# Kernel optimization log

Hardware: AMD Instinct MI355X
Metric: run time of the kernel (lower is better)

The kernel has to match this reference:

```python
import jax, jax.numpy as jnp
import numpy as np

BUCKETS = 256


def _gru_cell(x, h, W_ih, W_hh, b_ih, b_hh):
    # torch GRUCell math, gate order (r, z, n)
    gi = x @ W_ih.T + b_ih            # [B, 3H]
    gh = h @ W_hh.T + b_hh            # [B, 3H]
    i_r, i_z, i_n = jnp.split(gi, 3, axis=-1)
    h_r, h_z, h_n = jnp.split(gh, 3, axis=-1)
    r = jax.nn.sigmoid(i_r + h_r)
    z = jax.nn.sigmoid(i_z + h_z)
    n = jnp.tanh(i_n + r * h_n)
    return (1.0 - z) * n + z * h


def setup_inputs() -> dict:
    key = jax.random.key(0)
    ks = jax.random.split(key, 10)
    B, T, C, G, H, V = 16, 2000, 128, 512, 512, BUCKETS
    s = 0.1  # keep gates in a sane range
    return {
        "cond": jax.random.normal(ks[0], (B, T, C), jnp.float32),
        "h0": jnp.zeros((B, G), jnp.float32),
        "W_ih": jax.random.normal(ks[1], (3 * G, C), jnp.float32) * s,
        "W_hh": jax.random.normal(ks[2], (3 * G, G), jnp.float32) * s,
        "b_ih": jax.random.normal(ks[3], (3 * G,), jnp.float32) * s,
        "b_hh": jax.random.normal(ks[4], (3 * G,), jnp.float32) * s,
        "W_hid": jax.random.normal(ks[5], (H, G), jnp.float32) * s,
        "b_hid": jax.random.normal(ks[6], (H,), jnp.float32) * s,
        "W_out": jax.random.normal(ks[7], (V, H), jnp.float32) * s,
        "b_out": jax.random.normal(ks[8], (V,), jnp.float32) * s,
        "embedding": jax.random.normal(ks[9], (V, C), jnp.float32) * s,
    }


def reference(cond, h0, W_ih, W_hh, b_ih, b_hh, W_hid, b_hid, W_out, b_out, embedding):
    B, T, C = cond.shape
    keys = jax.random.split(jax.random.key(1), T)
    prev0 = jnp.full((B,), BUCKETS // 2, jnp.int32)  # mid-bucket = mu-law zero

    def step(carry, inp):
        h, prev = carry
        cond_t, k = inp
        x = cond_t + embedding[prev]                  # [B, C]
        h = _gru_cell(x, h, W_ih, W_hh, b_ih, b_hh)   # [B, G]
        hid = jax.nn.relu(h @ W_hid.T + b_hid)        # [B, H]
        logits = hid @ W_out.T + b_out                # [B, V]
        sample = jax.random.categorical(k, logits, axis=-1).astype(jnp.int32)
        return (h, sample), (logits, sample)

    (h_final, _), (logits, samples) = jax.lax.scan(
        step, (h0, prev0), (jnp.swapaxes(cond, 0, 1), keys))
    # logits: [T, B, V] -> [B, T, V]; samples: [T, B] -> [B, T]
    return jnp.swapaxes(logits, 0, 1), jnp.swapaxes(samples, 0, 1), h_final
```

## Files before the change

kernel.cpp:

```cpp
#include <hip/hip_runtime.h>
#include <stdint.h>
#include <math.h>

#define NBLK 128
#define NTHR 256
#define Bn 16
#define Tn 2000
#define Cn 128
#define Gn 512
#define Hn 512
#define Vn 256

#define WS_DBL_BASE 512
#define GRP_STRIDE  3072

#define OUT_SAMP ((size_t)Bn*Tn*Vn)
#define OUT_HF   (OUT_SAMP + (size_t)Bn*Tn)

typedef __attribute__((ext_vector_type(2))) double d2_t;

__device__ __forceinline__ unsigned rotl32(unsigned v, int n) {
  return (v << n) | (v >> (32 - n));
}

__device__ __forceinline__ void threefry2x32(unsigned k0, unsigned k1,
                                             unsigned c0, unsigned c1,
                                             unsigned& o0, unsigned& o1) {
  unsigned ks2 = k0 ^ k1 ^ 0x1BD11BDAu;
  unsigned x0 = c0 + k0;
  unsigned x1 = c1 + k1;
#define TF_R(r) { x0 += x1; x1 = rotl32(x1, r); x1 ^= x0; }
  TF_R(13) TF_R(15) TF_R(26) TF_R(6)
  x0 += k1;  x1 += ks2 + 1u;
  TF_R(17) TF_R(29) TF_R(16) TF_R(24)
  x0 += ks2; x1 += k0 + 2u;
  TF_R(13) TF_R(15) TF_R(26) TF_R(6)
  x0 += k0;  x1 += k1 + 3u;
  TF_R(17) TF_R(29) TF_R(16) TF_R(24)
  x0 += k1;  x1 += ks2 + 4u;
  TF_R(13) TF_R(15) TF_R(26) TF_R(6)
  x0 += ks2; x1 += k0 + 5u;
#undef TF_R
  o0 = x0; o1 = x1;
}

__device__ __forceinline__ void st_d(double* p, double v) {
  asm volatile("global_store_dwordx2 %0, %1, off sc0 sc1"
               :: "v"(p), "v"(v) : "memory");
}
__device__ __forceinline__ d2_t ld_d2(const double* p) {
  d2_t r;
  asm volatile("global_load_dwordx4 %0, %1, off sc0 sc1\n\t"
               "s_waitcnt vmcnt(0)" : "=v"(r) : "v"(p));
  return r;
}
__device__ __forceinline__ void ld8(const double* pl, int v, double* o) {
  const double* a0 = pl + v;
  const double* a1 = pl + 512 + v;
  const double* a2 = pl + 1024 + v;
  const double* a3 = pl + 1536 + v;
  double o0, o1, o2, o3, o4, o5, o6, o7;
  asm volatile(
    "global_load_dwordx2 %[r0], %[p0], off sc0 sc1\n\t"
    "global_load_dwordx2 %[r1], %[p0], off offset:2048 sc0 sc1\n\t"
    "global_load_dwordx2 %[r2], %[p1], off sc0 sc1\n\t"
    "global_load_dwordx2 %[r3], %[p1], off offset:2048 sc0 sc1\n\t"
    "global_load_dwordx2 %[r4], %[p2], off sc0 sc1\n\t"
    "global_load_dwordx2 %[r5], %[p2], off offset:2048 sc0 sc1\n\t"
    "global_load_dwordx2 %[r6], %[p3], off sc0 sc1\n\t"
    "global_load_dwordx2 %[r7], %[p3], off offset:2048 sc0 sc1\n\t"
    "s_waitcnt vmcnt(0)"
    : [r0]"=v"(o0), [r1]"=v"(o1), [r2]"=v"(o2), [r3]"=v"(o3),
      [r4]"=v"(o4), [r5]"=v"(o5), [r6]"=v"(o6), [r7]"=v"(o7)
    : [p0]"v"(a0), [p1]"v"(a1), [p2]"v"(a2), [p3]"v"(a3));
  o[0]=o0; o[1]=o1; o[2]=o2; o[3]=o3; o[4]=o4; o[5]=o5; o[6]=o6; o[7]=o7;
}
__device__ __forceinline__ unsigned ld_u(const unsigned* p) {
  unsigned r;
  asm volatile("global_load_dword %0, %1, off sc0 sc1\n\t"
               "s_waitcnt vmcnt(0)" : "=v"(r) : "v"(p) : "memory");
  return r;
}
__device__ __forceinline__ void st_u(unsigned* p, unsigned v) {
  asm volatile("global_store_dword %0, %1, off sc0 sc1"
               :: "v"(p), "v"(v) : "memory");
}

__device__ __forceinline__ void gar(unsigned* flags, int slot, unsigned target) {
  asm volatile("s_waitcnt vmcnt(0)" ::: "memory");
  __syncthreads();
  if (threadIdx.x == 0) st_u(&flags[slot], target);
}
__device__ __forceinline__ void gwt(unsigned* flags, unsigned target) {
  if (threadIdx.x < 8) {
    int guard = 0;
    while (ld_u(&flags[threadIdx.x]) < target) {
      if (++guard > 5000000) break;
    }
  }
  asm volatile("" ::: "memory");
  __syncthreads();
}

extern "C" __global__ __launch_bounds__(NTHR)
void wavernn_groups(const float* __restrict__ cond, const float* __restrict__ h0,
                    const float* __restrict__ W_ih, const float* __restrict__ W_hh,
                    const float* __restrict__ b_ih, const float* __restrict__ b_hh,
                    const float* __restrict__ W_hid, const float* __restrict__ b_hid,
                    const float* __restrict__ W_out, const float* __restrict__ b_out,
                    const float* __restrict__ emb,
                    float* __restrict__ out, double* __restrict__ ws) {
  const int tid = threadIdx.x;
  const int blk = blockIdx.x;
  const int g = blk >> 3;
  const int j = blk & 7;

  unsigned* flags = ((unsigned*)ws) + (size_t)g * 64;
  double* G   = ws + WS_DBL_BASE + (size_t)g * GRP_STRIDE;
  double* Hb0 = G;
  double* Hb1 = G + 512;
  double* PL  = G + 1024;

  __shared__ __attribute__((aligned(32))) double s_x[Cn];
  __shared__ __attribute__((aligned(32))) double s_h[Gn];
  __shared__ __attribute__((aligned(32))) double s_hid[64];
  __shared__ double s_r[64], s_z[64], s_hn[64], s_in[64];
  __shared__ double s_part[4][64];
  __shared__ double s_pv[4];
  __shared__ int    s_pi[4];

  if (tid < 64) st_d(&Hb0[j * 64 + tid],
                     (double)h0[(size_t)g * Gn + j * 64 + tid]);
  if (tid < Cn) s_x[tid] = (double)cond[(size_t)g * Tn * Cn + tid]
                         + (double)emb[128 * Cn + tid];
  unsigned pc = 1;
  gar(flags, j, pc); gwt(flags, pc); pc++;

  for (int t = 0; t < Tn; ++t) {
    double* hcur = (t & 1) ? Hb1 : Hb0;
    double* hnxt = (t & 1) ? Hb0 : Hb1;

    ((d2_t*)s_h)[tid] = ld_d2(hcur + 2 * tid);
    __syncthreads();
    {
      const int part = tid >> 6, gl = tid & 63;
      const double4* x4 = (const double4*)s_x;
      const double4* h4 = (const double4*)s_h;
      if (part <= 1) {
        const int row = part * 512 + j * 64 + gl;
        const float4* wi = (const float4*)(W_ih + (size_t)row * Cn);
        const float4* wh = (const float4*)(W_hh + (size_t)row * Gn);
        double a0 = 0., a1 = 0., a2 = 0., a3 = 0.;
#pragma unroll 8
        for (int k = 0; k < Cn / 4; ++k) {
          float4 w = wi[k]; double4 xv = x4[k];
          a0 = fma((double)w.x, xv.x, a0); a1 = fma((double)w.y, xv.y, a1);
          a2 = fma((double)w.z, xv.z, a2); a3 = fma((double)w.w, xv.w, a3);
        }
#pragma unroll 8
        for (int k = 0; k < Gn / 4; ++k) {
          float4 w = wh[k]; double4 hv = h4[k];
          a0 = fma((double)w.x, hv.x, a0); a1 = fma((double)w.y, hv.y, a1);
          a2 = fma((double)w.z, hv.z, a2); a3 = fma((double)w.w, hv.w, a3);
        }
        double pre = ((a0 + a1) + (a2 + a3)) + (double)b_ih[row] + (double)b_hh[row];
        double sig = 1.0 / (1.0 + exp(-pre));
        if (part == 0) s_r[gl] = sig; else s_z[gl] = sig;
      } else if (part == 2) {
        const int row = 1024 + j * 64 + gl;
        const float4* wh = (const float4*)(W_hh + (size_t)row * Gn);
        double a0 = 0., a1 = 0., a2 = 0., a3 = 0.;
#pragma unroll 8
        for (int k = 0; k < Gn / 4; ++k) {
          float4 w = wh[k]; double4 hv = h4[k];
          a0 = fma((double)w.x, hv.x, a0); a1 = fma((double)w.y, hv.y, a1);
          a2 = fma((double)w.z, hv.z, a2); a3 = fma((double)w.w, hv.w, a3);
        }
        s_hn[gl] = ((a0 + a1) + (a2 + a3)) + (double)b_hh[row];
      } else {
        const int row = 1024 + j * 64 + gl;
        const float4* wi = (const float4*)(W_ih + (size_t)row * Cn);
        double a0 = 0., a1 = 0., a2 = 0., a3 = 0.;
#pragma unroll 8
        for (int k = 0; k < Cn / 4; ++k) {
          float4 w = wi[k]; double4 xv = x4[k];
          a0 = fma((double)w.x, xv.x, a0); a1 = fma((double)w.y, xv.y, a1);
          a2 = fma((double)w.z, xv.z, a2); a3 = fma((double)w.w, xv.w, a3);
        }
        s_in[gl] = ((a0 + a1) + (a2 + a3)) + (double)b_ih[row];
      }
    }
    __syncthreads();
    if (tid < 64) {
      double r = s_r[tid], z = s_z[tid];
      double n = tanh(s_in[tid] + r * s_hn[tid]);
      double hv = (1.0 - z) * n + z * s_h[j * 64 + tid];
      st_d(&hnxt[j * 64 + tid], hv);
    }
    gar(flags, j, pc);
    float cond_next = 0.f;
    if (t + 1 < Tn && tid < Cn)
      cond_next = cond[((size_t)g * Tn + (t + 1)) * Cn + tid];
    unsigned kt0, kt1;
    threefry2x32(0u, 1u, 0u, (unsigned)t, kt0, kt1);
    gwt(flags, pc); pc++;

    ((d2_t*)s_h)[tid] = ld_d2(hnxt + 2 * tid);
    __syncthreads();
    if (t == Tn - 1 && j == 0) {
      out[OUT_HF + (size_t)g * Gn + tid] = (float)s_h[tid];
      out[OUT_HF + (size_t)g * Gn + tid + 256] = (float)s_h[tid + 256];
    }
    {
      const int row = j * 64 + (tid & 63);
      const int q = tid >> 6;
      const float4* wr = (const float4*)(W_hid + (size_t)row * Gn + q * 128);
      const double4* hh = (const double4*)(s_h + q * 128);
      double a0 = 0., a1 = 0., a2 = 0., a3 = 0.;
#pragma unroll 8
      for (int k = 0; k < 32; ++k) {
        float4 w = wr[k]; double4 hv = hh[k];
        a0 = fma((double)w.x, hv.x, a0); a1 = fma((double)w.y, hv.y, a1);
        a2 = fma((double)w.z, hv.z, a2); a3 = fma((double)w.w, hv.w, a3);
      }
      s_part[q][tid & 63] = (a0 + a1) + (a2 + a3);
    }
    __syncthreads();
    if (tid < 64) {
      double acc = (s_part[0][tid] + s_part[1][tid])
                 + (s_part[2][tid] + s_part[3][tid])
                 + (double)b_hid[j * 64 + tid];
      s_hid[tid] = acc > 0.0 ? acc : 0.0;
    }
    __syncthreads();
    {
      const int v = tid;
      const float4* wr = (const float4*)(W_out + (size_t)v * Hn + j * 64);
      const double4* hh = (const double4*)s_hid;
      double a0 = 0., a1 = 0., a2 = 0., a3 = 0.;
#pragma unroll 8
      for (int k = 0; k < 16; ++k) {
        float4 w = wr[k]; double4 hv = hh[k];
        a0 = fma((double)w.x, hv.x, a0); a1 = fma((double)w.y, hv.y, a1);
        a2 = fma((double)w.z, hv.z, a2); a3 = fma((double)w.w, hv.w, a3);
      }
      st_d(&PL[j * 256 + v], (a0 + a1) + (a2 + a3));
    }
    gar(flags, j, pc);
    double gum;
    {
      unsigned r0, r1;
      threefry2x32(kt0, kt1, 0u, (unsigned)(g * Vn + tid), r0, r1);
      unsigned bits = r0 ^ r1;
      float uf = __uint_as_float((bits >> 9) | 0x3f800000u) - 1.0f;
      if (uf <= 0.f) uf = 1.17549435e-38f;
      gum = -log(-log((double)uf));
    }
    gwt(flags, pc); pc++;

    int samp;
    {
      const int v = tid;
      double l[8];
      ld8(PL, v, l);
      double logit = ((((((((l[0] + l[1]) + l[2]) + l[3]) + l[4]) + l[5])
                       + l[6]) + l[7])) + (double)b_out[v];
      if (j == 0)
        out[(size_t)g * Tn * Vn + (size_t)t * Vn + v] = (float)logit;

      double bv = logit + gum;
      int bi = v;
#pragma unroll
      for (int off = 1; off < 64; off <<= 1) {
        double ov = __shfl_xor(bv, off, 64);
        int oi = __shfl_xor(bi, off, 64);
        if (ov > bv || (ov == bv && oi < bi)) { bv = ov; bi = oi; }
      }
      if ((tid & 63) == 0) { s_pv[tid >> 6] = bv; s_pi[tid >> 6] = bi; }
      __syncthreads();
      double fv = s_pv[0]; int fi = s_pi[0];
#pragma unroll
      for (int w = 1; w < 4; ++w) {
        double ov = s_pv[w]; int oi = s_pi[w];
        if (ov > fv || (ov == fv && oi < fi)) { fv = ov; fi = oi; }
      }
      samp = fi;
    }
    if (tid == 0 && j == 0) out[OUT_SAMP + (size_t)g * Tn + t] = (float)samp;
    if (t + 1 < Tn && tid < Cn) {
      s_x[tid] = (double)cond_next + (double)emb[(size_t)samp * Cn + tid];
    }
  }
}

extern "C" void kernel_launch(void* const* d_in, const int* in_sizes, int n_in,
                              void* d_out, int out_size, void* d_ws, size_t ws_size,
                              hipStream_t stream) {
  const float* cond  = (const float*)d_in[0];
  const float* h0    = (const float*)d_in[1];
  const float* W_ih  = (const float*)d_in[2];
  const float* W_hh  = (const float*)d_in[3];
  const float* b_ih  = (const float*)d_in[4];
  const float* b_hh  = (const float*)d_in[5];
  const float* W_hid = (const float*)d_in[6];
  const float* b_hid = (const float*)d_in[7];
  const float* W_out = (const float*)d_in[8];
  const float* b_out = (const float*)d_in[9];
  const float* emb   = (const float*)d_in[10];

  hipMemsetAsync(d_ws, 0, 4096, stream);
  hipLaunchKernelGGL(wavernn_groups, dim3(NBLK), dim3(NTHR), 0, stream,
                     cond, h0, W_ih, W_hh, b_ih, b_hh, W_hid, b_hid,
                     W_out, b_out, emb, (float*)d_out, (double*)d_ws);
}
```

Measured before the change: 51.33 ms.

## Overlap recurrent W_hh matvec with cross-block logit barrier wait

Restructures the per-step schedule so the h-dependent W_hh matvec for step t runs before waiting on the logits/sampling barrier of step t-1. The input-side W_ih work, which needs the sample, is deferred until after that wait. Meanwhile an idle wave prefetches the next cond row and computes Gumbel noise. The aim is to hide the inter-block barrier latency and the sampling latency behind useful matvec work on the serial critical path. The cost is more complex flag sequencing and a peeled epilogue for the final step's sampling.

```diff
diff --git a/kernel.cpp b/kernel.cpp
--- a/kernel.cpp
+++ b/kernel.cpp
@@ -42,6 +42,16 @@
   x0 += ks2; x1 += k0 + 5u;
 #undef TF_R
   o0 = x0; o1 = x1;
+}
+
+__device__ __forceinline__ double jax_gumbel(unsigned kt0, unsigned kt1,
+                                             unsigned f) {
+  unsigned r0, r1;
+  threefry2x32(kt0, kt1, 0u, f, r0, r1);
+  unsigned bits = r0 ^ r1;
+  float uf = __uint_as_float((bits >> 9) | 0x3f800000u) - 1.0f;
+  if (uf <= 0.f) uf = 1.17549435e-38f;
+  return -log(-log((double)uf));
 }
 
 __device__ __forceinline__ void st_d(double* p, double v) {
@@ -103,17 +113,18 @@
 }
 
 extern "C" __global__ __launch_bounds__(NTHR)
-void wavernn_groups(const float* __restrict__ cond, const float* __restrict__ h0,
-                    const float* __restrict__ W_ih, const float* __restrict__ W_hh,
-                    const float* __restrict__ b_ih, const float* __restrict__ b_hh,
-                    const float* __restrict__ W_hid, const float* __restrict__ b_hid,
-                    const float* __restrict__ W_out, const float* __restrict__ b_out,
-                    const float* __restrict__ emb,
-                    float* __restrict__ out, double* __restrict__ ws) {
+void wavernn_pipe(const float* __restrict__ cond, const float* __restrict__ h0,
+                  const float* __restrict__ W_ih, const float* __restrict__ W_hh,
+                  const float* __restrict__ b_ih, const float* __restrict__ b_hh,
+                  const float* __restrict__ W_hid, const float* __restrict__ b_hid,
+                  const float* __restrict__ W_out, const float* __restrict__ b_out,
+                  const float* __restrict__ emb,
+                  float* __restrict__ out, double* __restrict__ ws) {
   const int tid = threadIdx.x;
   const int blk = blockIdx.x;
   const int g = blk >> 3;
   const int j = blk & 7;
+  const int lane = tid & 63, wv = tid >> 6;
 
   unsigned* flags = ((unsigned*)ws) + (size_t)g * 64;
   double* G   = ws + WS_DBL_BASE + (size_t)g * GRP_STRIDE;
@@ -124,8 +135,10 @@
   __shared__ __attribute__((aligned(32))) double s_x[Cn];
   __shared__ __attribute__((aligned(32))) double s_h[Gn];
   __shared__ __attribute__((aligned(32))) double s_hid[64];
-  __shared__ double s_r[64], s_z[64], s_hn[64], s_in[64];
+  __shared__ double s_hn[64], s_in[64], s_z[64];
   __shared__ double s_part[4][64];
+  __shared__ double s_gum[256];
+  __shared__ float  s_cond[Cn];
   __shared__ double s_pv[4];
   __shared__ int    s_pi[4];
 
@@ -133,142 +146,51 @@
                      (double)h0[(size_t)g * Gn + j * 64 + tid]);
   if (tid < Cn) s_x[tid] = (double)cond[(size_t)g * Tn * Cn + tid]
                          + (double)emb[128 * Cn + tid];
-  unsigned pc = 1;
-  gar(flags, j, pc); gwt(flags, pc); pc++;
+  gar(flags, j, 1u); gwt(flags, 1u);
+  ((d2_t*)s_h)[tid] = ld_d2(Hb0 + 2 * tid);
+  __syncthreads();
 
   for (int t = 0; t < Tn; ++t) {
-    double* hcur = (t & 1) ? Hb1 : Hb0;
     double* hnxt = (t & 1) ? Hb0 : Hb1;
 
-    ((d2_t*)s_h)[tid] = ld_d2(hcur + 2 * tid);
-    __syncthreads();
-    {
-      const int part = tid >> 6, gl = tid & 63;
-      const double4* x4 = (const double4*)s_x;
+    double ha0 = 0., ha1 = 0., ha2 = 0., ha3 = 0.;
+    if (wv <= 2) {
+      const int row = wv * 512 + j * 64 + lane;
+      const float4* wh = (const float4*)(W_hh + (size_t)row * Gn);
       const double4* h4 = (const double4*)s_h;
-      if (part <= 1) {
-        const int row = part * 512 + j * 64 + gl;
-        const float4* wi = (const float4*)(W_ih + (size_t)row * Cn);
-        const float4* wh = (const float4*)(W_hh + (size_t)row * Gn);
-        double a0 = 0., a1 = 0., a2 = 0., a3 = 0.;
-#pragma unroll 8
-        for (int k = 0; k < Cn / 4; ++k) {
-          float4 w = wi[k]; double4 xv = x4[k];
-          a0 = fma((double)w.x, xv.x, a0); a1 = fma((double)w.y, xv.y, a1);
-          a2 = fma((double)w.z, xv.z, a2); a3 = fma((double)w.w, xv.w, a3);
+#pragma unroll 8
+      for (int k = 0; k < Gn / 4; ++k) {
+        float4 w = wh[k]; double4 hv = h4[k];
+        ha0 = fma((double)w.x, hv.x, ha0); ha1 = fma((double)w.y, hv.y, ha1);
+        ha2 = fma((double)w.z, hv.z, ha2); ha3 = fma((double)w.w, hv.w, ha3);
+      }
+      if (wv == 2)
+        s_hn[lane] = ((ha0 + ha1) + (ha2 + ha3)) + (double)b_hh[row];
+    } else {
+      const int c0 = 2 * lane;
+      s_cond[c0]     = cond[((size_t)g * Tn + t) * Cn + c0];
+      s_cond[c0 + 1] = cond[((size_t)g * Tn + t) * Cn + c0 + 1];
+      if (t > 0) {
+        unsigned kt0, kt1;
+        threefry2x32(0u, 1u, 0u, (unsigned)(t - 1), kt0, kt1);
+#pragma unroll
+        for (int i = 0; i < 4; ++i) {
+          int v = 4 * lane + i;
+          s_gum[v] = jax_gumbel(kt0, kt1, (unsigned)(g * Vn + v));
         }
-#pragma unroll 8
-        for (int k = 0; k < Gn / 4; ++k) {
-          float4 w = wh[k]; double4 hv = h4[k];
-          a0 = fma((double)w.x, hv.x, a0); a1 = fma((double)w.y, hv.y, a1);
-          a2 = fma((double)w.z, hv.z, a2); a3 = fma((double)w.w, hv.w, a3);
-        }
-        double pre = ((a0 + a1) + (a2 + a3)) + (double)b_ih[row] + (double)b_hh[row];
-        double sig = 1.0 / (1.0 + exp(-pre));
-        if (part == 0) s_r[gl] = sig; else s_z[gl] = sig;
-      } else if (part == 2) {
-        const int row = 1024 + j * 64 + gl;
-        const float4* wh = (const float4*)(W_hh + (size_t)row * Gn);
-        double a0 = 0., a1 = 0., a2 = 0., a3 = 0.;
-#pragma unroll 8
-        for (int k = 0; k < Gn / 4; ++k) {
-          float4 w = wh[k]; double4 hv = h4[k];
-          a0 = fma((double)w.x, hv.x, a0); a1 = fma((double)w.y, hv.y, a1);
-          a2 = fma((double)w.z, hv.z, a2); a3 = fma((double)w.w, hv.w, a3);
-        }
-        s_hn[gl] = ((a0 + a1) + (a2 + a3)) + (double)b_hh[row];
-      } else {
-        const int row = 1024 + j * 64 + gl;
-        const float4* wi = (const float4*)(W_ih + (size_t)row * Cn);
-        double a0 = 0., a1 = 0., a2 = 0., a3 = 0.;
-#pragma unroll 8
-        for (int k = 0; k < Cn / 4; ++k) {
-          float4 w = wi[k]; double4 xv = x4[k];
-          a0 = fma((double)w.x, xv.x, a0); a1 = fma((double)w.y, xv.y, a1);
-          a2 = fma((double)w.z, xv.z, a2); a3 = fma((double)w.w, xv.w, a3);
-        }
-        s_in[gl] = ((a0 + a1) + (a2 + a3)) + (double)b_ih[row];
-      }
-    }
-    __syncthreads();
-    if (tid < 64) {
-      double r = s_r[tid], z = s_z[tid];
-      double n = tanh(s_in[tid] + r * s_hn[tid]);
-      double hv = (1.0 - z) * n + z * s_h[j * 64 + tid];
-      st_d(&hnxt[j * 64 + tid], hv);
-    }
-    gar(flags, j, pc);
-    float cond_next = 0.f;
-    if (t + 1 < Tn && tid < Cn)
-      cond_next = cond[((size_t)g * Tn + (t + 1)) * Cn + tid];
-    unsigned kt0, kt1;
-    threefry2x32(0u, 1u, 0u, (unsigned)t, kt0, kt1);
-    gwt(flags, pc); pc++;
-
-    ((d2_t*)s_h)[tid] = ld_d2(hnxt + 2 * tid);
-    __syncthreads();
-    if (t == Tn - 1 && j == 0) {
-      out[OUT_HF + (size_t)g * Gn + tid] = (float)s_h[tid];
-      out[OUT_HF + (size_t)g * Gn + tid + 256] = (float)s_h[tid + 256];
-    }
-    {
-      const int row = j * 64 + (tid & 63);
-      const int q = tid >> 6;
-      const float4* wr = (const float4*)(W_hid + (size_t)row * Gn + q * 128);
-      const double4* hh = (const double4*)(s_h + q * 128);
-      double a0 = 0., a1 = 0., a2 = 0., a3 = 0.;
-#pragma unroll 8
-      for (int k = 0; k < 32; ++k) {
-        float4 w = wr[k]; double4 hv = hh[k];
-        a0 = fma((double)w.x, hv.x, a0); a1 = fma((double)w.y, hv.y, a1);
-        a2 = fma((double)w.z, hv.z, a2); a3 = fma((double)w.w, hv.w, a3);
-      }
-      s_part[q][tid & 63] = (a0 + a1) + (a2 + a3);
-    }
-    __syncthreads();
-    if (tid < 64) {
-      double acc = (s_part[0][tid] + s_part[1][tid])
-                 + (s_part[2][tid] + s_part[3][tid])
-                 + (double)b_hid[j * 64 + tid];
-      s_hid[tid] = acc > 0.0 ? acc : 0.0;
-    }
-    __syncthreads();
-    {
-      const int v = tid;
-      const float4* wr = (const float4*)(W_out + (size_t)v * Hn + j * 64);
-      const double4* hh = (const double4*)s_hid;
-      double a0 = 0., a1 = 0., a2 = 0., a3 = 0.;
-#pragma unroll 8
-      for (int k = 0; k < 16; ++k) {
-        float4 w = wr[k]; double4 hv = hh[k];
-        a0 = fma((double)w.x, hv.x, a0); a1 = fma((double)w.y, hv.y, a1);
-        a2 = fma((double)w.z, hv.z, a2); a3 = fma((double)w.w, hv.w, a3);
-      }
-      st_d(&PL[j * 256 + v], (a0 + a1) + (a2 + a3));
-    }
-    gar(flags, j, pc);
-    double gum;
-    {
-      unsigned r0, r1;
-      threefry2x32(kt0, kt1, 0u, (unsigned)(g * Vn + tid), r0, r1);
-      unsigned bits = r0 ^ r1;
-      float uf = __uint_as_float((bits >> 9) | 0x3f800000u) - 1.0f;
-      if (uf <= 0.f) uf = 1.17549435e-38f;
-      gum = -log(-log((double)uf));
-    }
-    gwt(flags, pc); pc++;
-
-    int samp;
-    {
+      }
+    }
+
+    if (t > 0) {
+      gwt(flags, (unsigned)(2 * t + 1));
       const int v = tid;
       double l[8];
       ld8(PL, v, l);
       double logit = ((((((((l[0] + l[1]) + l[2]) + l[3]) + l[4]) + l[5])
                        + l[6]) + l[7])) + (double)b_out[v];
       if (j == 0)
-        out[(size_t)g * Tn * Vn + (size_t)t * Vn + v] = (float)logit;
-
-      double bv = logit + gum;
+        out[(size_t)g * Tn * Vn + (size_t)(t - 1) * Vn + v] = (float)logit;
+      double bv = logit + s_gum[v];
       int bi = v;
 #pragma unroll
       for (int off = 1; off < 64; off <<= 1) {
@@ -276,7 +198,7 @@
         int oi = __shfl_xor(bi, off, 64);
         if (ov > bv || (ov == bv && oi < bi)) { bv = ov; bi = oi; }
       }
-      if ((tid & 63) == 0) { s_pv[tid >> 6] = bv; s_pi[tid >> 6] = bi; }
+      if (lane == 0) { s_pv[wv] = bv; s_pi[wv] = bi; }
       __syncthreads();
       double fv = s_pv[0]; int fi = s_pi[0];
 #pragma unroll
@@ -284,12 +206,130 @@
         double ov = s_pv[w]; int oi = s_pi[w];
         if (ov > fv || (ov == fv && oi < fi)) { fv = ov; fi = oi; }
       }
-      samp = fi;
-    }
-    if (tid == 0 && j == 0) out[OUT_SAMP + (size_t)g * Tn + t] = (float)samp;
-    if (t + 1 < Tn && tid < Cn) {
-      s_x[tid] = (double)cond_next + (double)emb[(size_t)samp * Cn + tid];
-    }
+      const int samp = fi;
+      if (tid == 0 && j == 0)
+        out[OUT_SAMP + (size_t)g * Tn + (t - 1)] = (float)samp;
+      if (tid < Cn)
+        s_x[tid] = (double)s_cond[tid] + (double)emb[(size_t)samp * Cn + tid];
+      __syncthreads();
+    } else {
+      __syncthreads();
+    }
+
+    double r_reg = 0.;
+    if (wv <= 1) {
+      const int row = wv * 512 + j * 64 + lane;
+      const float4* wi = (const float4*)(W_ih + (size_t)row * Cn);
+      const double4* x4 = (const double4*)s_x;
+      double xa0 = 0., xa1 = 0., xa2 = 0., xa3 = 0.;
+#pragma unroll 8
+      for (int k = 0; k < Cn / 4; ++k) {
+        float4 w = wi[k]; double4 xv = x4[k];
+        xa0 = fma((double)w.x, xv.x, xa0); xa1 = fma((double)w.y, xv.y, xa1);
+        xa2 = fma((double)w.z, xv.z, xa2); xa3 = fma((double)w.w, xv.w, xa3);
+      }
+      double gi = ((xa0 + xa1) + (xa2 + xa3)) + (double)b_ih[row];
+      double gh = ((ha0 + ha1) + (ha2 + ha3)) + (double)b_hh[row];
+      double pre = gi + gh;
+      double sig = 1.0 / (1.0 + exp(-pre));
+      if (wv == 0) r_reg = sig; else s_z[lane] = sig;
+    } else if (wv == 3) {
+      const int row = 1024 + j * 64 + lane;
+      const float4* wi = (const float4*)(W_ih + (size_t)row * Cn);
+      const double4* x4 = (const double4*)s_x;
+      double a0 = 0., a1 = 0., a2 = 0., a3 = 0.;
+#pragma unroll 8
+      for (int k = 0; k < Cn / 4; ++k) {
+        float4 w = wi[k]; double4 xv = x4[k];
+        a0 = fma((double)w.x, xv.x, a0); a1 = fma((double)w.y, xv.y, a1);
+        a2 = fma((double)w.z, xv.z, a2); a3 = fma((double)w.w, xv.w, a3);
+      }
+      s_in[lane] = ((a0 + a1) + (a2 + a3)) + (double)b_ih[row];
+    }
+    __syncthreads();
+
+    if (wv == 0) {
+      double z = s_z[lane];
+      double n = tanh(s_in[lane] + r_reg * s_hn[lane]);
+      double hv = (1.0 - z) * n + z * s_h[j * 64 + lane];
+      st_d(&hnxt[j * 64 + lane], hv);
+    }
+    gar(flags, j, (unsigned)(2 * t + 2));
+    gwt(flags, (unsigned)(2 * t + 2));
+    ((d2_t*)s_h)[tid] = ld_d2(hnxt + 2 * tid);
+    __syncthreads();
+    if (t == Tn - 1 && j == 0) {
+      out[OUT_HF + (size_t)g * Gn + tid] = (float)s_h[tid];
+      out[OUT_HF + (size_t)g * Gn + tid + 256] = (float)s_h[tid + 256];
+    }
+
+    {
+      const int row = j * 64 + lane;
+      const float4* wr = (const float4*)(W_hid + (size_t)row * Gn + wv * 128);
+      const double4* hh = (const double4*)(s_h + wv * 128);
+      double a0 = 0., a1 = 0., a2 = 0., a3 = 0.;
+#pragma unroll 8
+      for (int k = 0; k < 32; ++k) {
+        float4 w = wr[k]; double4 hv = hh[k];
+        a0 = fma((double)w.x, hv.x, a0); a1 = fma((double)w.y, hv.y, a1);
+        a2 = fma((double)w.z, hv.z, a2); a3 = fma((double)w.w, hv.w, a3);
+      }
+      s_part[wv][lane] = (a0 + a1) + (a2 + a3);
+    }
+    __syncthreads();
+    if (tid < 64) {
+      double acc = (s_part[0][tid] + s_part[1][tid])
+                 + (s_part[2][tid] + s_part[3][tid])
+                 + (double)b_hid[j * 64 + tid];
+      s_hid[tid] = acc > 0.0 ? acc : 0.0;
+    }
+    __syncthreads();
+    {
+      const int v = tid;
+      const float4* wr = (const float4*)(W_out + (size_t)v * Hn + j * 64);
+      const double4* hh = (const double4*)s_hid;
+      double a0 = 0., a1 = 0., a2 = 0., a3 = 0.;
+#pragma unroll 8
+      for (int k = 0; k < 16; ++k) {
+        float4 w = wr[k]; double4 hv = hh[k];
+        a0 = fma((double)w.x, hv.x, a0); a1 = fma((double)w.y, hv.y, a1);
+        a2 = fma((double)w.z, hv.z, a2); a3 = fma((double)w.w, hv.w, a3);
+      }
+      st_d(&PL[j * 256 + v], (a0 + a1) + (a2 + a3));
+    }
+    gar(flags, j, (unsigned)(2 * t + 3));
+  }
+
+  gwt(flags, (unsigned)(2 * Tn + 1));
+  {
+    const int v = tid;
+    double l[8];
+    ld8(PL, v, l);
+    double logit = ((((((((l[0] + l[1]) + l[2]) + l[3]) + l[4]) + l[5])
+                     + l[6]) + l[7])) + (double)b_out[v];
+    if (j == 0)
+      out[(size_t)g * Tn * Vn + (size_t)(Tn - 1) * Vn + v] = (float)logit;
+    unsigned kt0, kt1;
+    threefry2x32(0u, 1u, 0u, (unsigned)(Tn - 1), kt0, kt1);
+    double gum = jax_gumbel(kt0, kt1, (unsigned)(g * Vn + v));
+    double bv = logit + gum;
+    int bi = v;
+#pragma unroll
+    for (int off = 1; off < 64; off <<= 1) {
+      double ov = __shfl_xor(bv, off, 64);
+      int oi = __shfl_xor(bi, off, 64);
+      if (ov > bv || (ov == bv && oi < bi)) { bv = ov; bi = oi; }
+    }
+    if (lane == 0) { s_pv[wv] = bv; s_pi[wv] = bi; }
+    __syncthreads();
+    double fv = s_pv[0]; int fi = s_pi[0];
+#pragma unroll
+    for (int w = 1; w < 4; ++w) {
+      double ov = s_pv[w]; int oi = s_pi[w];
+      if (ov > fv || (ov == fv && oi < fi)) { fv = ov; fi = oi; }
+    }
+    if (tid == 0 && j == 0)
+      out[OUT_SAMP + (size_t)g * Tn + (Tn - 1)] = (float)fi;
   }
 }
 
@@ -309,7 +349,7 @@
   const float* emb   = (const float*)d_in[10];
 
   hipMemsetAsync(d_ws, 0, 4096, stream);
-  hipLaunchKernelGGL(wavernn_groups, dim3(NBLK), dim3(NTHR), 0, stream,
+  hipLaunchKernelGGL(wavernn_pipe, dim3(NBLK), dim3(NTHR), 0, stream,
                      cond, h0, W_ih, W_hh, b_ih, b_hh, W_hid, b_hid,
                      W_out, b_out, emb, (float*)d_out, (double*)d_ws);
 }
```

New measurement: 48.88 ms. 4.8% less time.
